# Kernel tuning notes

Measured on AMD Instinct MI355X. Metric: run time of the kernel, lower is better.

The kernel has to match this reference:

```python
import jax, jax.numpy as jnp
import numpy as np

ALPHA = 0.2  # leaky_relu negative slope
NEG_INF = -9e15


def _gat_stage(x, adj_mask, W, a):
    """Multi-head dense GAT layer (concat=True).
    x: [N, Fin], adj_mask: [N, N] bool, W: [H, Fin, O], a: [H, 2*O].
    Returns [N, H*O].
    """
    O = W.shape[-1]
    Wh = jnp.einsum('nf,hfo->hno', x, W)                 # [H, N, O]
    f1 = jnp.einsum('hno,ho->hn', Wh, a[:, :O])          # a_src . Wh_i
    f2 = jnp.einsum('hno,ho->hn', Wh, a[:, O:])          # a_dst . Wh_j
    e = f1[:, :, None] + f2[:, None, :]                  # [H, N, N]
    e = jnp.where(e > 0, e, ALPHA * e)                   # leaky_relu
    e = jnp.where(adj_mask[None], e, NEG_INF)            # mask non-edges
    att = jax.nn.softmax(e, axis=-1)                     # row softmax over neighbors
    h = jnp.einsum('hnm,hmo->hno', att, Wh)              # aggregate
    h = jax.nn.elu(h)                                    # concat=True -> elu
    H, N, _ = h.shape
    return jnp.transpose(h, (1, 0, 2)).reshape(N, H * O)  # head concat


def setup_inputs() -> dict:
    key = jax.random.key(0)
    ks = jax.random.split(key, 12)
    N, F0, NHID, H, NCLASS = 4096, 512, 64, 4, 40
    x = jax.random.normal(ks[0], (N, F0), jnp.float32)
    adj = jax.random.randint(ks[1], (N, N), 0, 2, jnp.int32)
    s = 0.05
    W1 = jax.random.normal(ks[2], (H, F0, NHID), jnp.float32) * s
    a1 = jax.random.normal(ks[3], (H, 2 * NHID), jnp.float32) * s
    W2 = jax.random.normal(ks[4], (4, H * NHID, 32), jnp.float32) * s
    a2 = jax.random.normal(ks[5], (4, 64), jnp.float32) * s
    W3 = jax.random.normal(ks[6], (4, 4 * 32, 16), jnp.float32) * s
    a3 = jax.random.normal(ks[7], (4, 32), jnp.float32) * s
    Wlin = jax.random.normal(ks[8], (4 * 16, NCLASS), jnp.float32) * s
    blin = jnp.zeros((NCLASS,), jnp.float32)
    return {"x": x, "adj": adj, "W1": W1, "a1": a1, "W2": W2, "a2": a2,
            "W3": W3, "a3": a3, "Wlin": Wlin, "blin": blin}


def reference(x, adj, W1, a1, W2, a2, W3, a3, Wlin, blin):
    # eval mode: all F.dropout calls are identity
    m = adj > 0
    h = _gat_stage(x, m, W1, a1)    # [N, 256]
    h = _gat_stage(h, m, W2, a2)    # [N, 128]
    h = _gat_stage(h, m, W3, a3)    # [N, 64]
    logits = h @ Wlin + blin        # [N, nclass]
    return jax.nn.log_softmax(logits, axis=1)
```

## Files before the change

kernel.cpp:

```cpp
#include <hip/hip_runtime.h>
#include <hip/hip_bf16.h>
#include <stdint.h>

typedef __attribute__((ext_vector_type(8))) short short8;
typedef __attribute__((ext_vector_type(4))) float float4v;

#define NHEADS 4
#define NNODES 4096
#define LOG2E 1.4426950408889634f
#define PSTR ((size_t)NHEADS * NNODES * 64)
#define LSTR ((size_t)NHEADS * NNODES)

__device__ __forceinline__ unsigned short f2b(float x) {
    union { float f; uint32_t u; } v; v.f = x;
    uint32_t u = v.u;
    uint32_t r = (u + 0x7FFFu + ((u >> 16) & 1u)) >> 16;
    return (unsigned short)r;
}
__device__ __forceinline__ float b2f(unsigned short s) {
    union { uint32_t u; float f; } v; v.u = ((uint32_t)s) << 16;
    return v.f;
}
__device__ __forceinline__ uint32_t cvtpk(float lo, float hi) {
    uint32_t r;
    asm("v_cvt_pk_bf16_f32 %0, %1, %2" : "=v"(r) : "v"(lo), "v"(hi));
    return r;
}

#define AS1 __attribute__((address_space(1)))
#define AS3 __attribute__((address_space(3)))
__device__ __forceinline__ void gl_lds16(const void* g, void* l) {
    __builtin_amdgcn_global_load_lds((const AS1 unsigned int*)g,
                                     (AS3 unsigned int*)l, 16, 0, 0);
}

__global__ __launch_bounds__(256) void k_pre(const int* __restrict__ adj,
                                             unsigned short* __restrict__ mask16,
                                             const float* __restrict__ x,
                                             unsigned short* __restrict__ xbf,
                                             const float* __restrict__ W1,
                                             unsigned short* __restrict__ WT1,
                                             const float* __restrict__ W2,
                                             unsigned short* __restrict__ WT2,
                                             const float* __restrict__ W3,
                                             unsigned short* __restrict__ WT3) {
    int b = blockIdx.x;
    if (b < 4096) {
        const int4* ap = (const int4*)(adj + ((size_t)b << 12)) + threadIdx.x * 4;
        int4 a0 = ap[0], a1 = ap[1], a2 = ap[2], a3 = ap[3];
        int v[16] = {a0.x, a0.y, a0.z, a0.w, a1.x, a1.y, a1.z, a1.w,
                     a2.x, a2.y, a2.z, a2.w, a3.x, a3.y, a3.z, a3.w};
        uint32_t bits = 0;
#pragma unroll
        for (int k = 0; k < 16; ++k) bits |= (uint32_t)(v[k] != 0) << k;
        mask16[(b << 8) + threadIdx.x] = (unsigned short)bits;
        return;
    }
    int i = (b - 4096) * 256 + threadIdx.x;
    if (i < 524288) {
        float4v v = ((const float4v*)x)[i];
        uint2 r;
        r.x = cvtpk(v[0], v[1]);
        r.y = cvtpk(v[2], v[3]);
        ((uint2*)xbf)[i] = r;
    } else if (i < 524288 + 131072) {
        int j = i - 524288;
        int o = j & 63, f = (j >> 6) & 511, h = j >> 15;
        WT1[((size_t)(h * 64 + o)) * 512 + f] = f2b(W1[j]);
    } else if (i < 524288 + 131072 + 32768) {
        int j = i - 655360;
        int o = j & 31, f = (j >> 5) & 255, h = j >> 13;
        WT2[((size_t)(h * 32 + o)) * 256 + f] = f2b(W2[j]);
    } else if (i < 524288 + 131072 + 32768 + 8192) {
        int j = i - 688128;
        int o = j & 15, f = (j >> 4) & 127, h = j >> 11;
        WT3[((size_t)(h * 16 + o)) * 128 + f] = f2b(W3[j]);
    }
}

template <int Fin, int O>
__global__ __launch_bounds__(256) void k_whgemm(const unsigned short* __restrict__ A,
                                                const unsigned short* __restrict__ WT,
                                                const float* __restrict__ avec,
                                                unsigned short* __restrict__ WhT,
                                                float* __restrict__ f1,
                                                float* __restrict__ f2) {
    __shared__ float scc[4][16][64];
    constexpr int HPB = 64 / O;
    const int rt = blockIdx.x & 255, cg = blockIdx.x >> 8;
    const int wv = threadIdx.x >> 6, lane = threadIdx.x & 63;
    const int il = lane & 15, g = lane >> 4;
    constexpr int kpw = Fin >> 2;
    const int k0 = wv * kpw;
    float4v acc[4];
#pragma unroll
    for (int ot = 0; ot < 4; ++ot) acc[ot] = (float4v){0.f, 0.f, 0.f, 0.f};
    const unsigned short* Arow = A + (size_t)(rt * 16 + il) * Fin + k0 + 8 * g;
    const unsigned short* Bcol = WT + (size_t)(cg * 64 + il) * Fin + k0 + 8 * g;
#pragma unroll
    for (int k = 0; k < kpw; k += 32) {
        short8 af = *(const short8*)(Arow + k);
#pragma unroll
        for (int ot = 0; ot < 4; ++ot) {
            short8 bf = *(const short8*)(Bcol + (size_t)ot * 16 * Fin + k);
            acc[ot] = __builtin_amdgcn_mfma_f32_16x16x32_bf16(af, bf, acc[ot], 0, 0, 0);
        }
    }
#pragma unroll
    for (int ot = 0; ot < 4; ++ot)
#pragma unroll
        for (int r = 0; r < 4; ++r) scc[wv][g * 4 + r][ot * 16 + il] = acc[ot][r];
    __syncthreads();
    for (int e = threadIdx.x; e < 1024; e += 256) {
        int row = e >> 6, col = e & 63;
        float v = scc[0][row][col] + scc[1][row][col] + scc[2][row][col] + scc[3][row][col];
        int gc = cg * 64 + col;
        int hh = gc / O, o = gc % O;
        WhT[((size_t)(hh * O + o)) * NNODES + rt * 16 + row] = f2b(v);
    }
    {
        int hl = lane / O, o = lane % O;
        int h = cg * HPB + hl;
        float av1 = avec[h * 2 * O + o];
        float av2 = avec[h * 2 * O + O + o];
#pragma unroll
        for (int r = 0; r < 4; ++r) {
            int row = wv * 4 + r;
            float v = scc[0][row][lane] + scc[1][row][lane] + scc[2][row][lane] + scc[3][row][lane];
            float s1 = v * av1, s2 = v * av2;
#pragma unroll
            for (int d = O / 2; d > 0; d >>= 1) {
                s1 += __shfl_xor(s1, d);
                s2 += __shfl_xor(s2, d);
            }
            if (o == 0) {
                int n = rt * 16 + row;
                f1[h * NNODES + n] = s1 * LOG2E;
                f2[h * NNODES + n] = s2 * LOG2E;
            }
        }
    }
}

template <int O>
__device__ __forceinline__ void stage_tile(const unsigned short* WB0, int j0,
                                           char* dst, int tid) {
    constexpr int CH = O * 8;
#pragma unroll
    for (int q = 0; q < CH; q += 256) {
        int s = q + tid;
        if (CH >= 256 || s < CH) {
            int o = s >> 3, c = s & 7;
            int cg = c ^ (o & 7);
            gl_lds16(WB0 + (size_t)o * NNODES + j0 + 8 * cg, dst + s * 16);
        }
    }
}

template <int O>
__global__ __launch_bounds__(256, 4) void k_pv(const uint32_t* __restrict__ mask,
                                               const float* __restrict__ f1L,
                                               const float* __restrict__ f2L,
                                               const unsigned short* __restrict__ WhT,
                                               float* __restrict__ pacc,
                                               float* __restrict__ lpart) {
    constexpr int NT = O / 16;
    constexpr int CH = O * 8;
    constexpr int LPT = (O == 64) ? 2 : 1;
    __shared__ unsigned short bt[3][CH * 8];
    __shared__ float sf2[1024];
    __shared__ uint32_t smask[64][34];
    const int b = blockIdx.x;
    const int js = b & 3, rt = (b >> 2) & 63, h = b >> 8;
    const int tid = threadIdx.x, wv = tid >> 6, lane = tid & 63;
    const int il = lane & 15, g = lane >> 4;
    const int j0b = js * 1024;
    const float* f2h = f2L + h * NNODES;
    const unsigned short* WB0 = WhT + (size_t)h * O * NNODES;
    const int nrow = wv * 16 + il;
    const float f1i = f1L[h * NNODES + rt * 64 + nrow];

    {
        int r = tid >> 2, c = (tid & 3) * 8;
        const uint32_t* mg = mask + (size_t)(rt * 64 + r) * 128 + js * 32 + c;
        uint4 m0 = *(const uint4*)mg;
        uint4 m1 = *(const uint4*)(mg + 4);
        asm volatile("s_waitcnt vmcnt(0)" ::: "memory");
        uint32_t* dstm = &smask[r][c];
        *(uint2*)(dstm + 0) = make_uint2(m0.x, m0.y);
        *(uint2*)(dstm + 2) = make_uint2(m0.z, m0.w);
        *(uint2*)(dstm + 4) = make_uint2(m1.x, m1.y);
        *(uint2*)(dstm + 6) = make_uint2(m1.z, m1.w);
    }
    gl_lds16(f2h + j0b + tid * 4, (char*)sf2 + tid * 16);
    stage_tile<O>(WB0, j0b, (char*)&bt[0][0], tid);
    stage_tile<O>(WB0, j0b + 64, (char*)&bt[1][0], tid);
    asm volatile("s_waitcnt vmcnt(%0) lgkmcnt(0)" :: "i"(LPT) : "memory");
    __builtin_amdgcn_sched_barrier(0);
    __builtin_amdgcn_s_barrier();

    float4v acc[NT];
#pragma unroll
    for (int ot = 0; ot < NT; ++ot) acc[ot] = (float4v){0.f, 0.f, 0.f, 0.f};
    float4v accl = (float4v){0.f, 0.f, 0.f, 0.f};
    short8 bones;
#pragma unroll
    for (int q = 0; q < 8; ++q) bones[q] = (il == 0) ? (short)0x3F80 : (short)0;

    auto compute = [&](int t, const char* btc) {
        uint2 mw = *(const uint2*)&smask[nrow][2 * t];
        const float* fp0 = sf2 + t * 64 + 8 * g;
#pragma unroll
        for (int s = 0; s < 2; ++s) {
            short8 B[NT];
#pragma unroll
            for (int ot = 0; ot < NT; ++ot) {
                int o = ot * 16 + il;
                B[ot] = *(const short8*)(btc + o * 128 + 16 * (((s << 2) + g) ^ (il & 7)));
            }
            const float* fp = fp0 + s * 32;
            float4v fa = *(const float4v*)fp;
            float4v fb = *(const float4v*)(fp + 4);
            uint32_t word = s ? mw.y : mw.x;
            uint32_t bits = (word >> (8 * g)) & 0xFFu;
            float p[8];
#pragma unroll
            for (int bb = 0; bb < 8; ++bb) {
                float sv = f1i + ((bb < 4) ? fa[bb] : fb[bb - 4]);
                sv = fmaxf(sv, 0.2f * sv);
                float pv = __builtin_amdgcn_exp2f(sv);
                p[bb] = ((bits >> bb) & 1u) ? pv : 0.f;
            }
            union { short8 s8; uint32_t u[4]; } pu;
            pu.u[0] = cvtpk(p[0], p[1]);
            pu.u[1] = cvtpk(p[2], p[3]);
            pu.u[2] = cvtpk(p[4], p[5]);
            pu.u[3] = cvtpk(p[6], p[7]);
#pragma unroll
            for (int ot = 0; ot < NT; ++ot)
                acc[ot] = __builtin_amdgcn_mfma_f32_16x16x32_bf16(pu.s8, B[ot], acc[ot], 0, 0, 0);
            accl = __builtin_amdgcn_mfma_f32_16x16x32_bf16(pu.s8, bones, accl, 0, 0, 0);
        }
    };

    for (int t = 0; t < 14; ++t) {
        stage_tile<O>(WB0, j0b + (t + 2) * 64, (char*)&bt[(t + 2) % 3][0], tid);
        compute(t, (const char*)&bt[t % 3][0]);
        asm volatile("s_waitcnt vmcnt(%0)" :: "i"(LPT) : "memory");
        __builtin_amdgcn_sched_barrier(0);
        __builtin_amdgcn_s_barrier();
    }
    compute(14, (const char*)&bt[2][0]);
    asm volatile("s_waitcnt vmcnt(0)" ::: "memory");
    __builtin_amdgcn_sched_barrier(0);
    __builtin_amdgcn_s_barrier();
    compute(15, (const char*)&bt[0][0]);

    float* pj = pacc + js * PSTR + (size_t)h * NNODES * O;
#pragma unroll
    for (int ot = 0; ot < NT; ++ot)
#pragma unroll
        for (int r = 0; r < 4; ++r)
            pj[(size_t)(rt * 64 + wv * 16 + g * 4 + r) * O + ot * 16 + il] = acc[ot][r];
    if (il == 0) {
        float* lj = lpart + js * LSTR + h * NNODES;
#pragma unroll
        for (int r = 0; r < 4; ++r)
            lj[rt * 64 + wv * 16 + g * 4 + r] = accl[r];
    }
}

template <int O>
__global__ __launch_bounds__(256) void k_fin(const float* __restrict__ pacc,
                                             const float* __restrict__ lpart,
                                             unsigned short* __restrict__ hout) {
    constexpr int HO = NHEADS * O;
    int e = blockIdx.x * 256 + threadIdx.x;
    int o = e % O;
    int n = (e / O) & (NNODES - 1);
    int h = e / (O * NNODES);
    size_t idx = ((size_t)h * NNODES + n) * O + o;
    float s = pacc[idx] + pacc[PSTR + idx] + pacc[2 * PSTR + idx] + pacc[3 * PSTR + idx];
    int li = h * NNODES + n;
    float l = lpart[li] + lpart[LSTR + li] + lpart[2 * LSTR + li] + lpart[3 * LSTR + li];
    float v = s / l;
    v = (v > 0.f) ? v : (__expf(v) - 1.f);
    hout[(size_t)n * HO + h * O + o] = f2b(v);
}

__global__ __launch_bounds__(256) void k_fin3final(const float* __restrict__ pacc,
                                                   const float* __restrict__ lpart,
                                                   const float* __restrict__ Wlin,
                                                   const float* __restrict__ blin,
                                                   float* __restrict__ out) {
    __shared__ float sh3[4][64];
    const int tid = threadIdx.x;
    const int n0 = blockIdx.x * 4;
    {
        int r = tid >> 6, hh = (tid >> 4) & 3, o = tid & 15;
        int n = n0 + r;
        size_t idx = ((size_t)hh * NNODES + n) * 16 + o;
        float s = pacc[idx] + pacc[PSTR + idx] + pacc[2 * PSTR + idx] + pacc[3 * PSTR + idx];
        int li = hh * NNODES + n;
        float l = lpart[li] + lpart[LSTR + li] + lpart[2 * LSTR + li] + lpart[3 * LSTR + li];
        float v = s / l;
        v = (v > 0.f) ? v : (__expf(v) - 1.f);
        sh3[r][hh * 16 + o] = v;
    }
    __syncthreads();
    int rr = tid >> 6, lane = tid & 63;
    int n = n0 + rr;
    float logit = 0.f;
    if (lane < 40) {
        logit = blin[lane];
#pragma unroll
        for (int k = 0; k < 64; ++k) logit += sh3[rr][k] * Wlin[k * 40 + lane];
    }
    float mv = (lane < 40) ? logit : -3.0e38f;
    for (int d = 32; d > 0; d >>= 1) mv = fmaxf(mv, __shfl_xor(mv, d));
    float ex = (lane < 40) ? __expf(logit - mv) : 0.f;
    for (int d = 32; d > 0; d >>= 1) ex += __shfl_xor(ex, d);
    if (lane < 40) out[n * 40 + lane] = logit - mv - logf(ex);
}

template <int Fin, int O>
static void run_stage(hipStream_t stream, const uint32_t* mask, const unsigned short* xin,
                      const unsigned short* WT, const float* avec,
                      unsigned short* WhT, float* f1, float* f2,
                      float* pacc, float* lpart) {
    constexpr int CG = (NHEADS * O) / 64;
    k_whgemm<Fin, O><<<256 * CG, 256, 0, stream>>>(xin, WT, avec, WhT, f1, f2);
    k_pv<O><<<1024, 256, 0, stream>>>(mask, f1, f2, WhT, pacc, lpart);
}

extern "C" void kernel_launch(void* const* d_in, const int* in_sizes, int n_in,
                              void* d_out, int out_size, void* d_ws, size_t ws_size,
                              hipStream_t stream) {
    const float* x    = (const float*)d_in[0];
    const int*   adj  = (const int*)d_in[1];
    const float* W1   = (const float*)d_in[2];
    const float* a1   = (const float*)d_in[3];
    const float* W2   = (const float*)d_in[4];
    const float* a2   = (const float*)d_in[5];
    const float* W3   = (const float*)d_in[6];
    const float* a3   = (const float*)d_in[7];
    const float* Wlin = (const float*)d_in[8];
    const float* blin = (const float*)d_in[9];
    float* out = (float*)d_out;

    char* ws = (char*)d_ws;
    uint32_t*       mask = (uint32_t*)ws;
    unsigned short* xbf  = (unsigned short*)(ws + (2u << 20));
    unsigned short* WhT  = (unsigned short*)(ws + (6u << 20));
    unsigned short* WT1  = (unsigned short*)(ws + (8u << 20));
    unsigned short* WT2  = (unsigned short*)(ws + (8u << 20) + (256u << 10));
    unsigned short* WT3  = (unsigned short*)(ws + (8u << 20) + (320u << 10));
    float*          f1   = (float*)(ws + (8u << 20) + (384u << 10));
    float*          f2   = (float*)(ws + (8u << 20) + (448u << 10));
    float*          lpart= (float*)(ws + (8u << 20) + (512u << 10));
    float*          pacc = (float*)(ws + (9u << 20));

    k_pre<<<4096 + 2720, 256, 0, stream>>>(adj, (unsigned short*)mask, x, xbf,
                                           W1, WT1, W2, WT2, W3, WT3);

    run_stage<512, 64>(stream, mask, xbf, WT1, a1, WhT, f1, f2, pacc, lpart);
    k_fin<64><<<NHEADS * NNODES * 64 / 256, 256, 0, stream>>>(pacc, lpart, xbf);
    run_stage<256, 32>(stream, mask, xbf, WT2, a2, WhT, f1, f2, pacc, lpart);
    k_fin<32><<<NHEADS * NNODES * 32 / 256, 256, 0, stream>>>(pacc, lpart, xbf);
    run_stage<128, 16>(stream, mask, xbf, WT3, a3, WhT, f1, f2, pacc, lpart);
    k_fin3final<<<NNODES / 4, 256, 0, stream>>>(pacc, lpart, Wlin, blin, out);
}
```

Baseline: 134.4 us.

## Split attention aggregation eight ways across keys and keep mask bits in registers

The key dimension of the P·V kernel is now split into 8 slices of 512 instead of 4 of 1024, doubling the grid to 2048 blocks and raising launch bounds to 5 blocks per CU. Each thread loads its own 16 mask words into registers instead of staging them through LDS. The O=16 stage uses 128-wide key tiles so each pipeline step does more work, with the LDS swizzle generalized to match. In exchange, the number of partial accumulators doubles, so the finalize kernels read twice as much pacc/lpart data and the workspace must hold 8 slices.

```diff
diff --git a/kernel.cpp b/kernel.cpp
--- a/kernel.cpp
+++ b/kernel.cpp
@@ -8,6 +8,7 @@
 #define NHEADS 4
 #define NNODES 4096
 #define LOG2E 1.4426950408889634f
+#define NJS 8
 #define PSTR ((size_t)NHEADS * NNODES * 64)
 #define LSTR ((size_t)NHEADS * NNODES)
 
@@ -143,59 +144,61 @@
 }
 
 template <int O>
-__device__ __forceinline__ void stage_tile(const unsigned short* WB0, int j0,
-                                           char* dst, int tid) {
-    constexpr int CH = O * 8;
-#pragma unroll
-    for (int q = 0; q < CH; q += 256) {
-        int s = q + tid;
-        if (CH >= 256 || s < CH) {
-            int o = s >> 3, c = s & 7;
-            int cg = c ^ (o & 7);
-            gl_lds16(WB0 + (size_t)o * NNODES + j0 + 8 * cg, dst + s * 16);
-        }
-    }
-}
-
-template <int O>
-__global__ __launch_bounds__(256, 4) void k_pv(const uint32_t* __restrict__ mask,
-                                               const float* __restrict__ f1L,
-                                               const float* __restrict__ f2L,
-                                               const unsigned short* __restrict__ WhT,
-                                               float* __restrict__ pacc,
-                                               float* __restrict__ lpart) {
-    constexpr int NT = O / 16;
-    constexpr int CH = O * 8;
-    constexpr int LPT = (O == 64) ? 2 : 1;
+__global__ __launch_bounds__(256, 5)
+void k_pv(const uint32_t* __restrict__ mask,
+          const float* __restrict__ f1L,
+          const float* __restrict__ f2L,
+          const unsigned short* __restrict__ WhT,
+          float* __restrict__ pacc,
+          float* __restrict__ lpart) {
+    constexpr int TJ  = (O == 16) ? 128 : 64;
+    constexpr int NTT = 512 / TJ;
+    constexpr int NT  = O / 16;
+    constexpr int CH  = O * TJ / 8;
+    constexpr int SPT = CH / 256;
+    constexpr int CPR = TJ / 8;
+    constexpr int NSUB = TJ / 32;
     __shared__ unsigned short bt[3][CH * 8];
-    __shared__ float sf2[1024];
-    __shared__ uint32_t smask[64][34];
+    __shared__ float sf2[512];
     const int b = blockIdx.x;
-    const int js = b & 3, rt = (b >> 2) & 63, h = b >> 8;
+    const int js = b & 7, rt = (b >> 3) & 63, h = b >> 9;
     const int tid = threadIdx.x, wv = tid >> 6, lane = tid & 63;
     const int il = lane & 15, g = lane >> 4;
-    const int j0b = js * 1024;
+    const int j0b = js * 512;
     const float* f2h = f2L + h * NNODES;
     const unsigned short* WB0 = WhT + (size_t)h * O * NNODES;
     const int nrow = wv * 16 + il;
+
     const float f1i = f1L[h * NNODES + rt * 64 + nrow];
-
+    const uint32_t* mrow = mask + (size_t)(rt * 64 + nrow) * 128 + js * 16;
+    uint32_t mw[16];
     {
-        int r = tid >> 2, c = (tid & 3) * 8;
-        const uint32_t* mg = mask + (size_t)(rt * 64 + r) * 128 + js * 32 + c;
-        uint4 m0 = *(const uint4*)mg;
-        uint4 m1 = *(const uint4*)(mg + 4);
-        asm volatile("s_waitcnt vmcnt(0)" ::: "memory");
-        uint32_t* dstm = &smask[r][c];
-        *(uint2*)(dstm + 0) = make_uint2(m0.x, m0.y);
-        *(uint2*)(dstm + 2) = make_uint2(m0.z, m0.w);
-        *(uint2*)(dstm + 4) = make_uint2(m1.x, m1.y);
-        *(uint2*)(dstm + 6) = make_uint2(m1.z, m1.w);
-    }
-    gl_lds16(f2h + j0b + tid * 4, (char*)sf2 + tid * 16);
-    stage_tile<O>(WB0, j0b, (char*)&bt[0][0], tid);
-    stage_tile<O>(WB0, j0b + 64, (char*)&bt[1][0], tid);
-    asm volatile("s_waitcnt vmcnt(%0) lgkmcnt(0)" :: "i"(LPT) : "memory");
+        uint4 a = *(const uint4*)(mrow);
+        uint4 c = *(const uint4*)(mrow + 4);
+        uint4 d = *(const uint4*)(mrow + 8);
+        uint4 e = *(const uint4*)(mrow + 12);
+        mw[0] = a.x;  mw[1] = a.y;  mw[2] = a.z;  mw[3] = a.w;
+        mw[4] = c.x;  mw[5] = c.y;  mw[6] = c.z;  mw[7] = c.w;
+        mw[8] = d.x;  mw[9] = d.y;  mw[10] = d.z; mw[11] = d.w;
+        mw[12] = e.x; mw[13] = e.y; mw[14] = e.z; mw[15] = e.w;
+    }
+    asm volatile("s_waitcnt vmcnt(0)" ::: "memory");
+    __builtin_amdgcn_sched_barrier(0);
+
+    auto stage_tile = [&](int t, int buf) {
+#pragma unroll
+        for (int q = 0; q < SPT; ++q) {
+            int s = q * 256 + tid;
+            int o = s / CPR, c = s % CPR;
+            int cs = c ^ (o & (CPR - 1));
+            gl_lds16(WB0 + (size_t)o * NNODES + j0b + t * TJ + 8 * cs,
+                     (char*)&bt[buf][0] + s * 16);
+        }
+    };
+    if (tid < 128) gl_lds16(f2h + j0b + tid * 4, (char*)sf2 + tid * 16);
+    stage_tile(0, 0);
+    stage_tile(1, 1);
+    asm volatile("s_waitcnt vmcnt(%0)" :: "i"(SPT) : "memory");
     __builtin_amdgcn_sched_barrier(0);
     __builtin_amdgcn_s_barrier();
 
@@ -207,21 +210,22 @@
 #pragma unroll
     for (int q = 0; q < 8; ++q) bones[q] = (il == 0) ? (short)0x3F80 : (short)0;
 
-    auto compute = [&](int t, const char* btc) {
-        uint2 mw = *(const uint2*)&smask[nrow][2 * t];
-        const float* fp0 = sf2 + t * 64 + 8 * g;
-#pragma unroll
-        for (int s = 0; s < 2; ++s) {
+    auto compute = [&](int t) {
+        const char* btc = (const char*)&bt[t % 3][0];
+        const float* fp0 = sf2 + t * TJ + 8 * g;
+#pragma unroll
+        for (int s = 0; s < NSUB; ++s) {
             short8 B[NT];
 #pragma unroll
             for (int ot = 0; ot < NT; ++ot) {
                 int o = ot * 16 + il;
-                B[ot] = *(const short8*)(btc + o * 128 + 16 * (((s << 2) + g) ^ (il & 7)));
+                B[ot] = *(const short8*)(btc + o * (CPR * 16) +
+                                         16 * (((s << 2) + g) ^ (o & (CPR - 1))));
             }
             const float* fp = fp0 + s * 32;
             float4v fa = *(const float4v*)fp;
             float4v fb = *(const float4v*)(fp + 4);
-            uint32_t word = s ? mw.y : mw.x;
+            uint32_t word = mw[t * NSUB + s];
             uint32_t bits = (word >> (8 * g)) & 0xFFu;
             float p[8];
 #pragma unroll
@@ -243,18 +247,19 @@
         }
     };
 
-    for (int t = 0; t < 14; ++t) {
-        stage_tile<O>(WB0, j0b + (t + 2) * 64, (char*)&bt[(t + 2) % 3][0], tid);
-        compute(t, (const char*)&bt[t % 3][0]);
-        asm volatile("s_waitcnt vmcnt(%0)" :: "i"(LPT) : "memory");
+#pragma unroll
+    for (int t = 0; t < NTT - 2; ++t) {
+        stage_tile(t + 2, (t + 2) % 3);
+        compute(t);
+        asm volatile("s_waitcnt vmcnt(%0)" :: "i"(SPT) : "memory");
         __builtin_amdgcn_sched_barrier(0);
         __builtin_amdgcn_s_barrier();
     }
-    compute(14, (const char*)&bt[2][0]);
+    compute(NTT - 2);
     asm volatile("s_waitcnt vmcnt(0)" ::: "memory");
     __builtin_amdgcn_sched_barrier(0);
     __builtin_amdgcn_s_barrier();
-    compute(15, (const char*)&bt[0][0]);
+    compute(NTT - 1);
 
     float* pj = pacc + js * PSTR + (size_t)h * NNODES * O;
 #pragma unroll
@@ -280,9 +285,13 @@
     int n = (e / O) & (NNODES - 1);
     int h = e / (O * NNODES);
     size_t idx = ((size_t)h * NNODES + n) * O + o;
-    float s = pacc[idx] + pacc[PSTR + idx] + pacc[2 * PSTR + idx] + pacc[3 * PSTR + idx];
     int li = h * NNODES + n;
-    float l = lpart[li] + lpart[LSTR + li] + lpart[2 * LSTR + li] + lpart[3 * LSTR + li];
+    float s = 0.f, l = 0.f;
+#pragma unroll
+    for (int k = 0; k < NJS; ++k) {
+        s += pacc[k * PSTR + idx];
+        l += lpart[k * LSTR + li];
+    }
     float v = s / l;
     v = (v > 0.f) ? v : (__expf(v) - 1.f);
     hout[(size_t)n * HO + h * O + o] = f2b(v);
@@ -300,9 +309,13 @@
         int r = tid >> 6, hh = (tid >> 4) & 3, o = tid & 15;
         int n = n0 + r;
         size_t idx = ((size_t)hh * NNODES + n) * 16 + o;
-        float s = pacc[idx] + pacc[PSTR + idx] + pacc[2 * PSTR + idx] + pacc[3 * PSTR + idx];
         int li = hh * NNODES + n;
-        float l = lpart[li] + lpart[LSTR + li] + lpart[2 * LSTR + li] + lpart[3 * LSTR + li];
+        float s = 0.f, l = 0.f;
+#pragma unroll
+        for (int k = 0; k < NJS; ++k) {
+            s += pacc[k * PSTR + idx];
+            l += lpart[k * LSTR + li];
+        }
         float v = s / l;
         v = (v > 0.f) ? v : (__expf(v) - 1.f);
         sh3[r][hh * 16 + o] = v;
@@ -330,7 +343,7 @@
                       float* pacc, float* lpart) {
     constexpr int CG = (NHEADS * O) / 64;
     k_whgemm<Fin, O><<<256 * CG, 256, 0, stream>>>(xin, WT, avec, WhT, f1, f2);
-    k_pv<O><<<1024, 256, 0, stream>>>(mask, f1, f2, WhT, pacc, lpart);
+    k_pv<O><<<4 * 64 * NJS, 256, 0, stream>>>(mask, f1, f2, WhT, pacc, lpart);
 }
 
 extern "C" void kernel_launch(void* const* d_in, const int* in_sizes, int n_in,
```

Measured after the change: 148.1 us. +10.2%, slower.

## Fuse split-K finalize and ELU into next stage's Wh GEMM prologue

Applied to the files above, without the earlier changes.

The separate k_fin kernels, which summed the partial attention accumulators, normalised, applied ELU and wrote bf16 activations, are removed. That work now runs in the prologue of the next layer's k_whgemm, which builds a swizzled bf16 A tile in shared memory. The change also fully unrolls the k_pv tile loop, drops the bounds guard in stage_tile, and fixes the swizzle XOR index to use o instead of il. It saves two kernel launches and a global round-trip of the activations, but each GEMM block now reads the pacc partials redundantly across its column-group blocks.

```diff
diff --git a/kernel.cpp b/kernel.cpp
--- a/kernel.cpp
+++ b/kernel.cpp
@@ -8,6 +8,7 @@
 #define NHEADS 4
 #define NNODES 4096
 #define LOG2E 1.4426950408889634f
+#define NJS 4
 #define PSTR ((size_t)NHEADS * NNODES * 64)
 #define LSTR ((size_t)NHEADS * NNODES)
 
@@ -16,10 +17,6 @@
     uint32_t u = v.u;
     uint32_t r = (u + 0x7FFFu + ((u >> 16) & 1u)) >> 16;
     return (unsigned short)r;
-}
-__device__ __forceinline__ float b2f(unsigned short s) {
-    union { uint32_t u; float f; } v; v.u = ((uint32_t)s) << 16;
-    return v.f;
 }
 __device__ __forceinline__ uint32_t cvtpk(float lo, float hi) {
     uint32_t r;
@@ -78,20 +75,55 @@
     }
 }
 
-template <int Fin, int O>
+template <int Fin, int O, int PO>
 __global__ __launch_bounds__(256) void k_whgemm(const unsigned short* __restrict__ A,
                                                 const unsigned short* __restrict__ WT,
                                                 const float* __restrict__ avec,
                                                 unsigned short* __restrict__ WhT,
                                                 float* __restrict__ f1,
-                                                float* __restrict__ f2) {
+                                                float* __restrict__ f2,
+                                                const float* __restrict__ pacc,
+                                                const float* __restrict__ lpart) {
     __shared__ float scc[4][16][64];
+    __shared__ unsigned short sa[(PO > 0) ? 16 * Fin : 1];
+    __shared__ float sl[(PO > 0) ? 64 : 1];
     constexpr int HPB = 64 / O;
     const int rt = blockIdx.x & 255, cg = blockIdx.x >> 8;
     const int wv = threadIdx.x >> 6, lane = threadIdx.x & 63;
     const int il = lane & 15, g = lane >> 4;
     constexpr int kpw = Fin >> 2;
     const int k0 = wv * kpw;
+
+    if constexpr (PO > 0) {
+        int t = threadIdx.x;
+        if (t < 64) {
+            int r = t >> 2, hh = t & 3;
+            int n = rt * 16 + r;
+            float l = 0.f;
+#pragma unroll
+            for (int k = 0; k < NJS; ++k) l += lpart[k * LSTR + hh * NNODES + n];
+            sl[r * 4 + hh] = l;
+        }
+        __syncthreads();
+        constexpr int EPT = 16 * Fin / 256;
+#pragma unroll
+        for (int q = 0; q < EPT; ++q) {
+            int e = q * 256 + t;
+            int r = e / Fin, f = e % Fin;
+            int hh = f / PO, o = f % PO;
+            int n = rt * 16 + r;
+            size_t idx = ((size_t)hh * NNODES + n) * PO + o;
+            float s = 0.f;
+#pragma unroll
+            for (int k = 0; k < NJS; ++k) s += pacc[k * PSTR + idx];
+            float v = s / sl[r * 4 + hh];
+            v = (v > 0.f) ? v : (__expf(v) - 1.f);
+            int c = f >> 3, pos = f & 7;
+            sa[r * Fin + ((c ^ (r & 7)) << 3) + pos] = f2b(v);
+        }
+        __syncthreads();
+    }
+
     float4v acc[4];
 #pragma unroll
     for (int ot = 0; ot < 4; ++ot) acc[ot] = (float4v){0.f, 0.f, 0.f, 0.f};
@@ -99,7 +131,13 @@
     const unsigned short* Bcol = WT + (size_t)(cg * 64 + il) * Fin + k0 + 8 * g;
 #pragma unroll
     for (int k = 0; k < kpw; k += 32) {
-        short8 af = *(const short8*)(Arow + k);
+        short8 af;
+        if constexpr (PO > 0) {
+            int ch = ((k0 + k) >> 3) + g;
+            af = *(const short8*)(sa + il * Fin + ((ch ^ (il & 7)) << 3));
+        } else {
+            af = *(const short8*)(Arow + k);
+        }
 #pragma unroll
         for (int ot = 0; ot < 4; ++ot) {
             short8 bf = *(const short8*)(Bcol + (size_t)ot * 16 * Fin + k);
@@ -148,12 +186,10 @@
     constexpr int CH = O * 8;
 #pragma unroll
     for (int q = 0; q < CH; q += 256) {
-        int s = q + tid;
-        if (CH >= 256 || s < CH) {
-            int o = s >> 3, c = s & 7;
-            int cg = c ^ (o & 7);
-            gl_lds16(WB0 + (size_t)o * NNODES + j0 + 8 * cg, dst + s * 16);
-        }
+        int s = (CH >= 256) ? (q + tid) : (tid & (CH - 1));
+        int o = s >> 3, c = s & 7;
+        int cg = c ^ (o & 7);
+        gl_lds16(WB0 + (size_t)o * NNODES + j0 + 8 * cg, dst + s * 16);
     }
 }
 
@@ -207,7 +243,8 @@
 #pragma unroll
     for (int q = 0; q < 8; ++q) bones[q] = (il == 0) ? (short)0x3F80 : (short)0;
 
-    auto compute = [&](int t, const char* btc) {
+    auto compute = [&](int t) {
+        const char* btc = (const char*)&bt[t % 3][0];
         uint2 mw = *(const uint2*)&smask[nrow][2 * t];
         const float* fp0 = sf2 + t * 64 + 8 * g;
 #pragma unroll
@@ -216,7 +253,7 @@
 #pragma unroll
             for (int ot = 0; ot < NT; ++ot) {
                 int o = ot * 16 + il;
-                B[ot] = *(const short8*)(btc + o * 128 + 16 * (((s << 2) + g) ^ (il & 7)));
+                B[ot] = *(const short8*)(btc + o * 128 + 16 * (((s << 2) + g) ^ (o & 7)));
             }
             const float* fp = fp0 + s * 32;
             float4v fa = *(const float4v*)fp;
@@ -243,18 +280,19 @@
         }
     };
 
+#pragma unroll
     for (int t = 0; t < 14; ++t) {
         stage_tile<O>(WB0, j0b + (t + 2) * 64, (char*)&bt[(t + 2) % 3][0], tid);
-        compute(t, (const char*)&bt[t % 3][0]);
+        compute(t);
         asm volatile("s_waitcnt vmcnt(%0)" :: "i"(LPT) : "memory");
         __builtin_amdgcn_sched_barrier(0);
         __builtin_amdgcn_s_barrier();
     }
-    compute(14, (const char*)&bt[2][0]);
+    compute(14);
     asm volatile("s_waitcnt vmcnt(0)" ::: "memory");
     __builtin_amdgcn_sched_barrier(0);
     __builtin_amdgcn_s_barrier();
-    compute(15, (const char*)&bt[0][0]);
+    compute(15);
 
     float* pj = pacc + js * PSTR + (size_t)h * NNODES * O;
 #pragma unroll
@@ -268,24 +306,6 @@
         for (int r = 0; r < 4; ++r)
             lj[rt * 64 + wv * 16 + g * 4 + r] = accl[r];
     }
-}
-
-template <int O>
-__global__ __launch_bounds__(256) void k_fin(const float* __restrict__ pacc,
-                                             const float* __restrict__ lpart,
-                                             unsigned short* __restrict__ hout) {
-    constexpr int HO = NHEADS * O;
-    int e = blockIdx.x * 256 + threadIdx.x;
-    int o = e % O;
-    int n = (e / O) & (NNODES - 1);
-    int h = e / (O * NNODES);
-    size_t idx = ((size_t)h * NNODES + n) * O + o;
-    float s = pacc[idx] + pacc[PSTR + idx] + pacc[2 * PSTR + idx] + pacc[3 * PSTR + idx];
-    int li = h * NNODES + n;
-    float l = lpart[li] + lpart[LSTR + li] + lpart[2 * LSTR + li] + lpart[3 * LSTR + li];
-    float v = s / l;
-    v = (v > 0.f) ? v : (__expf(v) - 1.f);
-    hout[(size_t)n * HO + h * O + o] = f2b(v);
 }
 
 __global__ __launch_bounds__(256) void k_fin3final(const float* __restrict__ pacc,
@@ -300,9 +320,13 @@
         int r = tid >> 6, hh = (tid >> 4) & 3, o = tid & 15;
         int n = n0 + r;
         size_t idx = ((size_t)hh * NNODES + n) * 16 + o;
-        float s = pacc[idx] + pacc[PSTR + idx] + pacc[2 * PSTR + idx] + pacc[3 * PSTR + idx];
         int li = hh * NNODES + n;
-        float l = lpart[li] + lpart[LSTR + li] + lpart[2 * LSTR + li] + lpart[3 * LSTR + li];
+        float s = 0.f, l = 0.f;
+#pragma unroll
+        for (int k = 0; k < NJS; ++k) {
+            s += pacc[k * PSTR + idx];
+            l += lpart[k * LSTR + li];
+        }
         float v = s / l;
         v = (v > 0.f) ? v : (__expf(v) - 1.f);
         sh3[r][hh * 16 + o] = v;
@@ -321,16 +345,6 @@
     float ex = (lane < 40) ? __expf(logit - mv) : 0.f;
     for (int d = 32; d > 0; d >>= 1) ex += __shfl_xor(ex, d);
     if (lane < 40) out[n * 40 + lane] = logit - mv - logf(ex);
-}
-
-template <int Fin, int O>
-static void run_stage(hipStream_t stream, const uint32_t* mask, const unsigned short* xin,
-                      const unsigned short* WT, const float* avec,
-                      unsigned short* WhT, float* f1, float* f2,
-                      float* pacc, float* lpart) {
-    constexpr int CG = (NHEADS * O) / 64;
-    k_whgemm<Fin, O><<<256 * CG, 256, 0, stream>>>(xin, WT, avec, WhT, f1, f2);
-    k_pv<O><<<1024, 256, 0, stream>>>(mask, f1, f2, WhT, pacc, lpart);
 }
 
 extern "C" void kernel_launch(void* const* d_in, const int* in_sizes, int n_in,
@@ -363,10 +377,14 @@
     k_pre<<<4096 + 2720, 256, 0, stream>>>(adj, (unsigned short*)mask, x, xbf,
                                            W1, WT1, W2, WT2, W3, WT3);
 
-    run_stage<512, 64>(stream, mask, xbf, WT1, a1, WhT, f1, f2, pacc, lpart);
-    k_fin<64><<<NHEADS * NNODES * 64 / 256, 256, 0, stream>>>(pacc, lpart, xbf);
-    run_stage<256, 32>(stream, mask, xbf, WT2, a2, WhT, f1, f2, pacc, lpart);
-    k_fin<32><<<NHEADS * NNODES * 32 / 256, 256, 0, stream>>>(pacc, lpart, xbf);
-    run_stage<128, 16>(stream, mask, xbf, WT3, a3, WhT, f1, f2, pacc, lpart);
+    k_whgemm<512, 64, 0><<<1024, 256, 0, stream>>>(xbf, WT1, a1, WhT, f1, f2,
+                                                   nullptr, nullptr);
+    k_pv<64><<<1024, 256, 0, stream>>>(mask, f1, f2, WhT, pacc, lpart);
+    k_whgemm<256, 32, 64><<<512, 256, 0, stream>>>(nullptr, WT2, a2, WhT, f1, f2,
+                                                   pacc, lpart);
+    k_pv<32><<<1024, 256, 0, stream>>>(mask, f1, f2, WhT, pacc, lpart);
+    k_whgemm<128, 16, 32><<<256, 256, 0, stream>>>(nullptr, WT3, a3, WhT, f1, f2,
+                                                   pacc, lpart);
+    k_pv<16><<<1024, 256, 0, stream>>>(mask, f1, f2, WhT, pacc, lpart);
     k_fin3final<<<NNODES / 4, 256, 0, stream>>>(pacc, lpart, Wlin, blin, out);
 }
```

Result: slower. 137.5 us (+2.3%).
